# Kernel optimization log

Hardware: AMD Instinct MI355X
Metric: run time of the kernel (lower is better)

Reference implementation:

```python
import jax, jax.numpy as jnp
import numpy as np
import math

IN_DIM, OUT_DIM, NUM_BASIS = 256, 128, 6
MAX_IN_SEQ, MAX_OUT_SEQ = 512, 256
REDUCTION = 2
LN_EPS = 1e-5


def setup_inputs() -> dict:
    key = jax.random.key(0)
    ks = jax.random.split(key, 8)
    u = lambda k, shape, a: jax.random.uniform(k, shape, jnp.float32, -a, a)
    x = jax.random.normal(ks[0], (16, MAX_IN_SEQ, IN_DIM), jnp.float32)
    M = u(ks[1], (OUT_DIM, IN_DIM), 0.5)
    P = u(ks[2], (OUT_DIM, OUT_DIM, NUM_BASIS), 0.1)
    Linker = u(ks[3], (MAX_IN_SEQ, MAX_OUT_SEQ), 0.1)
    ln_gamma = jnp.ones((OUT_DIM,), jnp.float32)
    ln_beta = jnp.zeros((OUT_DIM,), jnp.float32)
    res_W = u(ks[4], (OUT_DIM, IN_DIM), 0.1)
    res_linker = u(ks[5], (MAX_IN_SEQ, MAX_OUT_SEQ), 0.1)
    # periods[i,j,g] = i*(out_dim*num_basis) + j*num_basis + g + 2 (non-trainable buffer)
    periods = (jnp.arange(OUT_DIM * OUT_DIM * NUM_BASIS, dtype=jnp.float32)
               .reshape(OUT_DIM, OUT_DIM, NUM_BASIS) + 2.0)
    return {"x": x, "M": M, "P": P, "Linker": Linker, "ln_gamma": ln_gamma,
            "ln_beta": ln_beta, "res_W": res_W, "res_linker": res_linker,
            "periods": periods, "actual_seq_len": 512}


def _layer_norm(z, gamma, beta):
    mu = jnp.mean(z, axis=-1, keepdims=True)
    var = jnp.var(z, axis=-1, keepdims=True)
    return (z - mu) * jax.lax.rsqrt(var + LN_EPS) * gamma + beta


def reference(x, M, P, Linker, ln_gamma, ln_beta, res_W, res_linker, periods, actual_seq_len):
    b, seq_len, _ = x.shape
    # Z = LN(x @ M^T)
    Z = _layer_norm(jnp.matmul(x, M.T), ln_gamma, ln_beta)  # (b, s, out)
    # position-dependent trig basis: phi[s,i,j,g] = cos(2*pi*s / periods[i,j,g])
    k = jnp.arange(seq_len, dtype=jnp.float32)[:, None, None, None]
    phi = jnp.cos(2.0 * math.pi * k / periods[None])          # (s, out, out, nb)
    # fold basis into per-position mixing matrix, then contract (matches sum over dims 3,4)
    W = jnp.einsum('ijg,sijg->sij', P, phi)                   # (s, out, out)
    T = jnp.einsum('bsj,sij->bsi', Z, W)                      # (b, s, out)
    # adaptive linker: reduce sequence length
    L = actual_seq_len
    Lo = max(1, L // REDUCTION)
    U = jnp.einsum('bsi,so->boi', T[:, :L], Linker[:L, :Lo])  # (b, out_seq, out)
    # 'separate' residual
    rfeat = jnp.matmul(x[:, :L], res_W.T)                     # (b, s, out)
    residual = jnp.einsum('bsi,so->boi', rfeat, res_linker[:L, :Lo])
    return U + residual
```

## Files before the change

### kernel.cpp

```cpp
#include <hip/hip_runtime.h>
#include <hip/hip_bf16.h>

#define LN_EPS 1e-5f


typedef __attribute__((ext_vector_type(8))) short short8;
typedef __attribute__((ext_vector_type(4))) float floatx4;

__device__ __forceinline__ unsigned short f2bf(float f) {
    __hip_bfloat16 h = __float2bfloat16(f);
    union { __hip_bfloat16 h; unsigned short u; } v; v.h = h; return v.u;
}
__device__ __forceinline__ unsigned int pack2(float a, float b) {
    return (unsigned int)f2bf(a) | ((unsigned int)f2bf(b) << 16);
}
__device__ __forceinline__ short8 pack8(float4 a, float4 b) {
    union { short8 s; uint4 u; } v;
    v.u.x = pack2(a.x, a.y); v.u.y = pack2(a.z, a.w);
    v.u.z = pack2(b.x, b.y); v.u.w = pack2(b.z, b.w);
    return v.s;
}

union SMem {
    struct { float buf[32 * 258]; float red1[256]; float red2[256]; float mus[32]; float rsg[32]; } p1;
    struct { unsigned short axs[32 * 40]; unsigned short bs[256 * 40]; } stg;
    unsigned short lcat[32 * 260];
};

__global__ __launch_bounds__(256) void s1_produce(const float* __restrict__ x,
                                                  const float* __restrict__ M,
                                                  const float* __restrict__ resW,
                                                  const float* __restrict__ gamma,
                                                  const float* __restrict__ beta,
                                                  const float* __restrict__ P,
                                                  const float* __restrict__ periods,
                                                  const float* __restrict__ Linker,
                                                  const float* __restrict__ resL,
                                                  unsigned short* __restrict__ Z,
                                                  unsigned short* __restrict__ TRt,
                                                  unsigned short* __restrict__ W,
                                                  unsigned short* __restrict__ LcatT) {
    __shared__ SMem sm;
    int blk = blockIdx.x, t = threadIdx.x;
    int w = t >> 6, l = t & 63;
    int lane15 = l & 15, quad = l >> 4;

    if (blk < 512) {
        int et = blk & 31, sc = blk >> 5;
        int n0 = et * 512 + t * 2;
        int jj = n0 & 7, il = (n0 >> 3) & 15, kq = (n0 >> 7) & 15, ig = (n0 >> 11) & 7;
        int e0 = (ig * 16 + il) * 128 + kq * 8 + jj;
        const float* pp = P + (size_t)e0 * 6;
        float4 pa = *(const float4*)(pp);
        float4 pb = *(const float4*)(pp + 4);
        float4 pc = *(const float4*)(pp + 8);
        float pf[12] = { pa.x, pa.y, pa.z, pa.w, pb.x, pb.y, pb.z, pb.w, pc.x, pc.y, pc.z, pc.w };
        const float* qp = periods + (size_t)e0 * 6;
        float4 qa = *(const float4*)(qp);
        float4 qb = *(const float4*)(qp + 4);
        float4 qc = *(const float4*)(qp + 8);
        float iv[12] = { __builtin_amdgcn_rcpf(qa.x), __builtin_amdgcn_rcpf(qa.y),
                         __builtin_amdgcn_rcpf(qa.z), __builtin_amdgcn_rcpf(qa.w),
                         __builtin_amdgcn_rcpf(qb.x), __builtin_amdgcn_rcpf(qb.y),
                         __builtin_amdgcn_rcpf(qb.z), __builtin_amdgcn_rcpf(qb.w),
                         __builtin_amdgcn_rcpf(qc.x), __builtin_amdgcn_rcpf(qc.y),
                         __builtin_amdgcn_rcpf(qc.z), __builtin_amdgcn_rcpf(qc.w) };
        float s0f = (float)(sc * 32);
        float tc[12], cm1[12], cc[12];
        #pragma unroll
        for (int g = 0; g < 12; ++g) {
            tc[g]  = 2.0f * __builtin_amdgcn_cosf(iv[g]);
            cm1[g] = __builtin_amdgcn_cosf(__builtin_amdgcn_fractf(s0f * iv[g]));
            cc[g]  = __builtin_amdgcn_cosf(__builtin_amdgcn_fractf((s0f + 1.0f) * iv[g]));
        }
        #pragma unroll 4
        for (int ss = 0; ss < 32; ++ss) {
            float a0 = 0.f, a1 = 0.f;
            #pragma unroll
            for (int g = 0; g < 6; ++g)  a0 += pf[g] * cm1[g];
            #pragma unroll
            for (int g = 6; g < 12; ++g) a1 += pf[g] * cm1[g];
            int s = sc * 32 + ss;
            *(unsigned int*)(W + (size_t)s * 16384 + n0) = pack2(a0, a1);
            #pragma unroll
            for (int g = 0; g < 12; ++g) {
                float cn = fmaf(tc[g], cc[g], -cm1[g]);
                cm1[g] = cc[g]; cc[g] = cn;
            }
        }
    } else if (blk < 768) {
        int r0 = (blk - 512) * 32;
        int wco = w * 64;
        floatx4 acc[2][4] = {};
        for (int km = 0; km < 256; km += 32) {
            {
                int row = t >> 3, c4 = (t & 7) * 4;
                float4 v = *(const float4*)(x + (size_t)(r0 + row) * 256 + km + c4);
                uint2 u; u.x = pack2(v.x, v.y); u.y = pack2(v.z, v.w);
                *(uint2*)(sm.stg.axs + row * 40 + c4) = u;
            }
            #pragma unroll
            for (int q = 0; q < 8; ++q) {
                int idx = t + 256 * q;
                int row = idx >> 3, c4 = (idx & 7) * 4;
                const float* src = (row < 128) ? (M + (size_t)row * 256)
                                               : (resW + (size_t)(row - 128) * 256);
                float4 v = *(const float4*)(src + km + c4);
                uint2 u; u.x = pack2(v.x, v.y); u.y = pack2(v.z, v.w);
                *(uint2*)(sm.stg.bs + row * 40 + c4) = u;
            }
            __syncthreads();
            int k0 = quad * 8;
            short8 a0 = *(const short8*)(sm.stg.axs + lane15 * 40 + k0);
            short8 a1 = *(const short8*)(sm.stg.axs + (16 + lane15) * 40 + k0);
            #pragma unroll
            for (int nt = 0; nt < 4; ++nt) {
                short8 b = *(const short8*)(sm.stg.bs + (wco + nt * 16 + lane15) * 40 + k0);
                acc[0][nt] = __builtin_amdgcn_mfma_f32_16x16x32_bf16(a0, b, acc[0][nt], 0, 0, 0);
                acc[1][nt] = __builtin_amdgcn_mfma_f32_16x16x32_bf16(a1, b, acc[1][nt], 0, 0, 0);
            }
            __syncthreads();
        }
        #pragma unroll
        for (int mt = 0; mt < 2; ++mt)
            #pragma unroll
            for (int nt = 0; nt < 4; ++nt)
                #pragma unroll
                for (int r = 0; r < 4; ++r) {
                    int ro = mt * 16 + quad * 4 + r;
                    int co = w * 64 + nt * 16 + lane15;
                    sm.p1.buf[ro * 258 + co] = acc[mt][nt][r];
                }
        __syncthreads();
        {
            int r = t >> 3, seg = t & 7;
            float s1 = 0.f, s2 = 0.f;
            #pragma unroll
            for (int e = 0; e < 16; ++e) { float v = sm.p1.buf[r * 258 + seg * 16 + e]; s1 += v; s2 += v * v; }
            sm.p1.red1[r * 8 + seg] = s1; sm.p1.red2[r * 8 + seg] = s2;
        }
        __syncthreads();
        if (t < 32) {
            float s1 = 0.f, s2 = 0.f;
            #pragma unroll
            for (int e = 0; e < 8; ++e) { s1 += sm.p1.red1[t * 8 + e]; s2 += sm.p1.red2[t * 8 + e]; }
            float mu = s1 * (1.0f / 128.0f);
            float var = s2 * (1.0f / 128.0f) - mu * mu;
            sm.p1.mus[t] = mu; sm.p1.rsg[t] = rsqrtf(var + LN_EPS);
        }
        __syncthreads();
        int b = r0 >> 9, s0 = r0 & 511;
        {
            int r = t >> 3, c0 = (t & 7) * 16;
            int s_t = s0 + r;
            float mu = sm.p1.mus[r], rs = sm.p1.rsg[r];
            float zv[16];
            #pragma unroll
            for (int e = 0; e < 16; ++e) {
                int j = c0 + e;
                zv[e] = (sm.p1.buf[r * 258 + j] - mu) * rs * gamma[j] + beta[j];
            }
            uint4 oz0, oz1;
            oz0.x = pack2(zv[0], zv[1]);  oz0.y = pack2(zv[2], zv[3]);
            oz0.z = pack2(zv[4], zv[5]);  oz0.w = pack2(zv[6], zv[7]);
            oz1.x = pack2(zv[8], zv[9]);  oz1.y = pack2(zv[10], zv[11]);
            oz1.z = pack2(zv[12], zv[13]); oz1.w = pack2(zv[14], zv[15]);
            unsigned short* zdst = Z + (size_t)s_t * 2048 + (((c0 >> 3) * 16 + b) << 3);
            *(uint4*)(zdst) = oz0;
            *(uint4*)(zdst + 128) = oz1;
        }
        {
            int j = t >> 1, sh = (t & 1) * 16;
            unsigned int ow[8];
            #pragma unroll
            for (int p = 0; p < 8; ++p) {
                float v0 = sm.p1.buf[(sh + 2 * p) * 258 + 128 + j];
                float v1 = sm.p1.buf[(sh + 2 * p + 1) * 258 + 128 + j];
                ow[p] = pack2(v0, v1);
            }
            int kqA = 64 + ((s0 + sh) >> 3);
            unsigned short* dst = TRt + (size_t)b * 131072 + ((size_t)(kqA * 128 + j) << 3);
            uint4 u0; u0.x = ow[0]; u0.y = ow[1]; u0.z = ow[2]; u0.w = ow[3];
            uint4 u1; u1.x = ow[4]; u1.y = ow[5]; u1.z = ow[6]; u1.w = ow[7];
            *(uint4*)(dst) = u0;
            *(uint4*)(dst + 1024) = u1;
        }
    } else {
        int kb = blk - 768;
        int k0 = kb * 32;
        const float* src = (kb < 16) ? (Linker + (size_t)k0 * 256)
                                     : (resL + (size_t)(k0 - 512) * 256);
        #pragma unroll
        for (int q = 0; q < 8; ++q) {
            int lin = t + 256 * q;
            int row = lin >> 6, col4 = (lin & 63) * 4;
            float4 v = *(const float4*)(src + row * 256 + col4);
            *(unsigned int*)(sm.lcat + row * 260 + col4)     = pack2(v.x, v.y);
            *(unsigned int*)(sm.lcat + row * 260 + col4 + 2) = pack2(v.z, v.w);
        }
        __syncthreads();
        int o = t;
        unsigned int outw[16];
        #pragma unroll
        for (int kp = 0; kp < 16; ++kp) {
            unsigned int lo = sm.lcat[(2 * kp) * 260 + o];
            unsigned int hi = sm.lcat[(2 * kp + 1) * 260 + o];
            outw[kp] = lo | (hi << 16);
        }
        #pragma unroll
        for (int qq = 0; qq < 4; ++qq) {
            uint4 u; u.x = outw[qq*4]; u.y = outw[qq*4+1]; u.z = outw[qq*4+2]; u.w = outw[qq*4+3];
            *(uint4*)(LcatT + (((size_t)(kb * 4 + qq) * 256 + o) << 3)) = u;
        }
    }
}

__global__ __launch_bounds__(256) void k2b_t(const unsigned short* __restrict__ W,
                                             const unsigned short* __restrict__ Z,
                                             unsigned short* __restrict__ TRt) {
    __shared__ unsigned short tbuf[16 * 64 * 4];
    int t = threadIdx.x, w = t >> 6, l = t & 63;
    int lane15 = l & 15, quad = l >> 4;
    int st = blockIdx.x >> 1, ih = blockIdx.x & 1;
    int s0 = st * 4;
    int ig = ih * 4 + w;
    #pragma unroll
    for (int ss = 0; ss < 4; ++ss) {
        int s = s0 + ss;
        floatx4 acc = {};
        #pragma unroll
        for (int kk = 0; kk < 4; ++kk) {
            int kq = kk * 4 + quad;
            short8 a  = *(const short8*)(Z + (size_t)s * 2048 + ((kq * 16 + lane15) << 3));
            short8 bf = *(const short8*)(W + (size_t)s * 16384 + (((ig * 16 + kq) * 16 + lane15) << 3));
            acc = __builtin_amdgcn_mfma_f32_16x16x32_bf16(a, bf, acc, 0, 0, 0);
        }
        int il = w * 16 + lane15;
        #pragma unroll
        for (int r = 0; r < 4; ++r) {
            int brow = quad * 4 + r;
            tbuf[(brow * 64 + il) * 4 + ss] = f2bf(acc[r]);
        }
    }
    __syncthreads();
    int ihb = ih * 64;
    #pragma unroll
    for (int q = 0; q < 4; ++q) {
        int p = t + 256 * q;
        int b = p >> 6, il = p & 63;
        uint2 v = *(const uint2*)(tbuf + p * 4);
        *(uint2*)(TRt + (size_t)b * 131072 + (((s0 >> 3) * 128 + ihb + il) << 3) + (s0 & 7)) = v;
    }
}

__global__ __launch_bounds__(256) void k3_out(const unsigned short* __restrict__ LcatT,
                                              const unsigned short* __restrict__ TRt,
                                              float* __restrict__ out) {
    __shared__ float red[4 * 32 * 64];
    int t = threadIdx.x, w = t >> 6, l = t & 63;
    int lane15 = l & 15, quad = l >> 4;
    int b = blockIdx.x, o0 = blockIdx.y * 32, i0 = blockIdx.z * 64;
    const unsigned short* trb = TRt + (size_t)b * 131072;
    floatx4 acc[2][4] = {};
    #pragma unroll 2
    for (int kk = 0; kk < 8; ++kk) {
        int k0 = w * 256 + kk * 32 + quad * 8;
        int kq = k0 >> 3;
        short8 afr0 = *(const short8*)(LcatT + (((size_t)kq * 256 + o0 + lane15) << 3));
        short8 afr1 = *(const short8*)(LcatT + (((size_t)kq * 256 + o0 + 16 + lane15) << 3));
        #pragma unroll
        for (int nt = 0; nt < 4; ++nt) {
            short8 bfr = *(const short8*)(trb + (((size_t)kq * 128 + i0 + nt * 16 + lane15) << 3));
            acc[0][nt] = __builtin_amdgcn_mfma_f32_16x16x32_bf16(afr0, bfr, acc[0][nt], 0, 0, 0);
            acc[1][nt] = __builtin_amdgcn_mfma_f32_16x16x32_bf16(afr1, bfr, acc[1][nt], 0, 0, 0);
        }
    }
    #pragma unroll
    for (int mt = 0; mt < 2; ++mt)
        #pragma unroll
        for (int nt = 0; nt < 4; ++nt)
            #pragma unroll
            for (int r = 0; r < 4; ++r) {
                int ro = mt * 16 + quad * 4 + r;
                int co = nt * 16 + lane15;
                red[(w * 32 + ro) * 64 + co] = acc[mt][nt][r];
            }
    __syncthreads();
    {
        int ro = t >> 3, c0 = (t & 7) * 8;
        float vs[8];
        #pragma unroll
        for (int e = 0; e < 8; ++e) {
            float sum = 0.f;
            #pragma unroll
            for (int ww = 0; ww < 4; ++ww) sum += red[(ww * 32 + ro) * 64 + c0 + e];
            vs[e] = sum;
        }
        float4 o1 = { vs[0], vs[1], vs[2], vs[3] };
        float4 o2 = { vs[4], vs[5], vs[6], vs[7] };
        size_t ob = ((size_t)b * 256 + o0 + ro) * 128 + i0 + c0;
        *(float4*)(out + ob) = o1;
        *(float4*)(out + ob + 4) = o2;
    }
}

extern "C" void kernel_launch(void* const* d_in, const int* in_sizes, int n_in,
                              void* d_out, int out_size, void* d_ws, size_t ws_size,
                              hipStream_t stream) {
    const float* x      = (const float*)d_in[0];
    const float* M      = (const float*)d_in[1];
    const float* P      = (const float*)d_in[2];
    const float* Linker = (const float*)d_in[3];
    const float* gamma  = (const float*)d_in[4];
    const float* beta   = (const float*)d_in[5];
    const float* resW   = (const float*)d_in[6];
    const float* resL   = (const float*)d_in[7];
    const float* periods= (const float*)d_in[8];
    (void)in_sizes; (void)n_in; (void)out_size; (void)ws_size;

    float* ws = (float*)d_ws;
    unsigned short* LcatT = (unsigned short*)(ws);
    unsigned short* Z     = (unsigned short*)(ws + 131072);
    unsigned short* TRt   = (unsigned short*)(ws + 655360);
    unsigned short* W     = (unsigned short*)(ws + 1703936);

    s1_produce<<<800, 256, 0, stream>>>(x, M, resW, gamma, beta, P, periods,
                                        Linker, resL, Z, TRt, W, LcatT);
    k2b_t<<<256, 256, 0, stream>>>(W, Z, TRt);
    k3_out<<<dim3(16, 8, 2), 256, 0, stream>>>(LcatT, TRt, (float*)d_out);
}
```

Measured before the change: 106.8 us.

## Fuse three kernels into one cooperative megakernel with grid syncs

Merges the producer, T-computation and output kernels into a single cooperative launch of 512 blocks separated by grid-wide barriers. Roles are reassigned: 256 blocks do the LN matmul while the other 256 build the linker transpose and each compute two W tiles. The goal is to remove launch gaps and inter-kernel drain. In exchange it adds grid.sync costs, leaves half the blocks idle in the later phases, and serialises more W work per block.

```diff
diff --git a/kernel.cpp b/kernel.cpp
--- a/kernel.cpp
+++ b/kernel.cpp
@@ -1,5 +1,8 @@
 #include <hip/hip_runtime.h>
 #include <hip/hip_bf16.h>
+#include <hip/hip_cooperative_groups.h>
+
+namespace cg = cooperative_groups;
 
 #define LN_EPS 1e-5f
 
@@ -13,215 +16,203 @@
 }
 __device__ __forceinline__ unsigned int pack2(float a, float b) {
     return (unsigned int)f2bf(a) | ((unsigned int)f2bf(b) << 16);
-}
-__device__ __forceinline__ short8 pack8(float4 a, float4 b) {
-    union { short8 s; uint4 u; } v;
-    v.u.x = pack2(a.x, a.y); v.u.y = pack2(a.z, a.w);
-    v.u.z = pack2(b.x, b.y); v.u.w = pack2(b.z, b.w);
-    return v.s;
 }
 
 union SMem {
     struct { float buf[32 * 258]; float red1[256]; float red2[256]; float mus[32]; float rsg[32]; } p1;
     struct { unsigned short axs[32 * 40]; unsigned short bs[256 * 40]; } stg;
     unsigned short lcat[32 * 260];
+    unsigned short tbuf[16 * 64 * 4];
+    float red[4 * 32 * 64];
 };
 
-__global__ __launch_bounds__(256) void s1_produce(const float* __restrict__ x,
-                                                  const float* __restrict__ M,
-                                                  const float* __restrict__ resW,
-                                                  const float* __restrict__ gamma,
-                                                  const float* __restrict__ beta,
-                                                  const float* __restrict__ P,
-                                                  const float* __restrict__ periods,
-                                                  const float* __restrict__ Linker,
-                                                  const float* __restrict__ resL,
-                                                  unsigned short* __restrict__ Z,
-                                                  unsigned short* __restrict__ TRt,
-                                                  unsigned short* __restrict__ W,
-                                                  unsigned short* __restrict__ LcatT) {
-    __shared__ SMem sm;
-    int blk = blockIdx.x, t = threadIdx.x;
+__device__ void role_w(int vb, int t, const float* __restrict__ P,
+                       const float* __restrict__ periods, unsigned short* __restrict__ W) {
+    int et = vb & 31, sc = vb >> 5;
+    int n0 = et * 512 + t * 2;
+    int jj = n0 & 7, il = (n0 >> 3) & 15, kq = (n0 >> 7) & 15, ig = (n0 >> 11) & 7;
+    int e0 = (ig * 16 + il) * 128 + kq * 8 + jj;
+    const float* pp = P + (size_t)e0 * 6;
+    float4 pa = *(const float4*)(pp);
+    float4 pb = *(const float4*)(pp + 4);
+    float4 pc = *(const float4*)(pp + 8);
+    float pf[12] = { pa.x, pa.y, pa.z, pa.w, pb.x, pb.y, pb.z, pb.w, pc.x, pc.y, pc.z, pc.w };
+    const float* qp = periods + (size_t)e0 * 6;
+    float4 qa = *(const float4*)(qp);
+    float4 qb = *(const float4*)(qp + 4);
+    float4 qc = *(const float4*)(qp + 8);
+    float iv[12] = { __builtin_amdgcn_rcpf(qa.x), __builtin_amdgcn_rcpf(qa.y),
+                     __builtin_amdgcn_rcpf(qa.z), __builtin_amdgcn_rcpf(qa.w),
+                     __builtin_amdgcn_rcpf(qb.x), __builtin_amdgcn_rcpf(qb.y),
+                     __builtin_amdgcn_rcpf(qb.z), __builtin_amdgcn_rcpf(qb.w),
+                     __builtin_amdgcn_rcpf(qc.x), __builtin_amdgcn_rcpf(qc.y),
+                     __builtin_amdgcn_rcpf(qc.z), __builtin_amdgcn_rcpf(qc.w) };
+    float s0f = (float)(sc * 32);
+    float tc[12], cm1[12], cc[12];
+    #pragma unroll
+    for (int g = 0; g < 12; ++g) {
+        tc[g]  = 2.0f * __builtin_amdgcn_cosf(iv[g]);
+        cm1[g] = __builtin_amdgcn_cosf(__builtin_amdgcn_fractf(s0f * iv[g]));
+        cc[g]  = __builtin_amdgcn_cosf(__builtin_amdgcn_fractf((s0f + 1.0f) * iv[g]));
+    }
+    #pragma unroll 4
+    for (int ss = 0; ss < 32; ++ss) {
+        float a0 = 0.f, a1 = 0.f;
+        #pragma unroll
+        for (int g = 0; g < 6; ++g)  a0 += pf[g] * cm1[g];
+        #pragma unroll
+        for (int g = 6; g < 12; ++g) a1 += pf[g] * cm1[g];
+        int s = sc * 32 + ss;
+        *(unsigned int*)(W + (size_t)s * 16384 + n0) = pack2(a0, a1);
+        #pragma unroll
+        for (int g = 0; g < 12; ++g) {
+            float cn = fmaf(tc[g], cc[g], -cm1[g]);
+            cm1[g] = cc[g]; cc[g] = cn;
+        }
+    }
+}
+
+__device__ void role_k1(SMem& sm, int vb, int t,
+                        const float* __restrict__ x, const float* __restrict__ M,
+                        const float* __restrict__ resW, const float* __restrict__ gamma,
+                        const float* __restrict__ beta,
+                        unsigned short* __restrict__ Z, unsigned short* __restrict__ TRt) {
     int w = t >> 6, l = t & 63;
     int lane15 = l & 15, quad = l >> 4;
-
-    if (blk < 512) {
-        int et = blk & 31, sc = blk >> 5;
-        int n0 = et * 512 + t * 2;
-        int jj = n0 & 7, il = (n0 >> 3) & 15, kq = (n0 >> 7) & 15, ig = (n0 >> 11) & 7;
-        int e0 = (ig * 16 + il) * 128 + kq * 8 + jj;
-        const float* pp = P + (size_t)e0 * 6;
-        float4 pa = *(const float4*)(pp);
-        float4 pb = *(const float4*)(pp + 4);
-        float4 pc = *(const float4*)(pp + 8);
-        float pf[12] = { pa.x, pa.y, pa.z, pa.w, pb.x, pb.y, pb.z, pb.w, pc.x, pc.y, pc.z, pc.w };
-        const float* qp = periods + (size_t)e0 * 6;
-        float4 qa = *(const float4*)(qp);
-        float4 qb = *(const float4*)(qp + 4);
-        float4 qc = *(const float4*)(qp + 8);
-        float iv[12] = { __builtin_amdgcn_rcpf(qa.x), __builtin_amdgcn_rcpf(qa.y),
-                         __builtin_amdgcn_rcpf(qa.z), __builtin_amdgcn_rcpf(qa.w),
-                         __builtin_amdgcn_rcpf(qb.x), __builtin_amdgcn_rcpf(qb.y),
-                         __builtin_amdgcn_rcpf(qb.z), __builtin_amdgcn_rcpf(qb.w),
-                         __builtin_amdgcn_rcpf(qc.x), __builtin_amdgcn_rcpf(qc.y),
-                         __builtin_amdgcn_rcpf(qc.z), __builtin_amdgcn_rcpf(qc.w) };
-        float s0f = (float)(sc * 32);
-        float tc[12], cm1[12], cc[12];
-        #pragma unroll
-        for (int g = 0; g < 12; ++g) {
-            tc[g]  = 2.0f * __builtin_amdgcn_cosf(iv[g]);
-            cm1[g] = __builtin_amdgcn_cosf(__builtin_amdgcn_fractf(s0f * iv[g]));
-            cc[g]  = __builtin_amdgcn_cosf(__builtin_amdgcn_fractf((s0f + 1.0f) * iv[g]));
-        }
-        #pragma unroll 4
-        for (int ss = 0; ss < 32; ++ss) {
-            float a0 = 0.f, a1 = 0.f;
+    int r0 = vb * 32;
+    int wco = w * 64;
+    floatx4 acc[2][4] = {};
+    for (int km = 0; km < 256; km += 32) {
+        {
+            int row = t >> 3, c4 = (t & 7) * 4;
+            float4 v = *(const float4*)(x + (size_t)(r0 + row) * 256 + km + c4);
+            uint2 u; u.x = pack2(v.x, v.y); u.y = pack2(v.z, v.w);
+            *(uint2*)(sm.stg.axs + row * 40 + c4) = u;
+        }
+        #pragma unroll
+        for (int q = 0; q < 8; ++q) {
+            int idx = t + 256 * q;
+            int row = idx >> 3, c4 = (idx & 7) * 4;
+            const float* src = (row < 128) ? (M + (size_t)row * 256)
+                                           : (resW + (size_t)(row - 128) * 256);
+            float4 v = *(const float4*)(src + km + c4);
+            uint2 u; u.x = pack2(v.x, v.y); u.y = pack2(v.z, v.w);
+            *(uint2*)(sm.stg.bs + row * 40 + c4) = u;
+        }
+        __syncthreads();
+        int k0 = quad * 8;
+        short8 a0 = *(const short8*)(sm.stg.axs + lane15 * 40 + k0);
+        short8 a1 = *(const short8*)(sm.stg.axs + (16 + lane15) * 40 + k0);
+        #pragma unroll
+        for (int nt = 0; nt < 4; ++nt) {
+            short8 b = *(const short8*)(sm.stg.bs + (wco + nt * 16 + lane15) * 40 + k0);
+            acc[0][nt] = __builtin_amdgcn_mfma_f32_16x16x32_bf16(a0, b, acc[0][nt], 0, 0, 0);
+            acc[1][nt] = __builtin_amdgcn_mfma_f32_16x16x32_bf16(a1, b, acc[1][nt], 0, 0, 0);
+        }
+        __syncthreads();
+    }
+    #pragma unroll
+    for (int mt = 0; mt < 2; ++mt)
+        #pragma unroll
+        for (int nt = 0; nt < 4; ++nt)
             #pragma unroll
-            for (int g = 0; g < 6; ++g)  a0 += pf[g] * cm1[g];
-            #pragma unroll
-            for (int g = 6; g < 12; ++g) a1 += pf[g] * cm1[g];
-            int s = sc * 32 + ss;
-            *(unsigned int*)(W + (size_t)s * 16384 + n0) = pack2(a0, a1);
-            #pragma unroll
-            for (int g = 0; g < 12; ++g) {
-                float cn = fmaf(tc[g], cc[g], -cm1[g]);
-                cm1[g] = cc[g]; cc[g] = cn;
+            for (int r = 0; r < 4; ++r) {
+                int ro = mt * 16 + quad * 4 + r;
+                int co = w * 64 + nt * 16 + lane15;
+                sm.p1.buf[ro * 258 + co] = acc[mt][nt][r];
             }
-        }
-    } else if (blk < 768) {
-        int r0 = (blk - 512) * 32;
-        int wco = w * 64;
-        floatx4 acc[2][4] = {};
-        for (int km = 0; km < 256; km += 32) {
-            {
-                int row = t >> 3, c4 = (t & 7) * 4;
-                float4 v = *(const float4*)(x + (size_t)(r0 + row) * 256 + km + c4);
-                uint2 u; u.x = pack2(v.x, v.y); u.y = pack2(v.z, v.w);
-                *(uint2*)(sm.stg.axs + row * 40 + c4) = u;
-            }
-            #pragma unroll
-            for (int q = 0; q < 8; ++q) {
-                int idx = t + 256 * q;
-                int row = idx >> 3, c4 = (idx & 7) * 4;
-                const float* src = (row < 128) ? (M + (size_t)row * 256)
-                                               : (resW + (size_t)(row - 128) * 256);
-                float4 v = *(const float4*)(src + km + c4);
-                uint2 u; u.x = pack2(v.x, v.y); u.y = pack2(v.z, v.w);
-                *(uint2*)(sm.stg.bs + row * 40 + c4) = u;
-            }
-            __syncthreads();
-            int k0 = quad * 8;
-            short8 a0 = *(const short8*)(sm.stg.axs + lane15 * 40 + k0);
-            short8 a1 = *(const short8*)(sm.stg.axs + (16 + lane15) * 40 + k0);
-            #pragma unroll
-            for (int nt = 0; nt < 4; ++nt) {
-                short8 b = *(const short8*)(sm.stg.bs + (wco + nt * 16 + lane15) * 40 + k0);
-                acc[0][nt] = __builtin_amdgcn_mfma_f32_16x16x32_bf16(a0, b, acc[0][nt], 0, 0, 0);
-                acc[1][nt] = __builtin_amdgcn_mfma_f32_16x16x32_bf16(a1, b, acc[1][nt], 0, 0, 0);
-            }
-            __syncthreads();
-        }
-        #pragma unroll
-        for (int mt = 0; mt < 2; ++mt)
-            #pragma unroll
-            for (int nt = 0; nt < 4; ++nt)
-                #pragma unroll
-                for (int r = 0; r < 4; ++r) {
-                    int ro = mt * 16 + quad * 4 + r;
-                    int co = w * 64 + nt * 16 + lane15;
-                    sm.p1.buf[ro * 258 + co] = acc[mt][nt][r];
-                }
-        __syncthreads();
-        {
-            int r = t >> 3, seg = t & 7;
-            float s1 = 0.f, s2 = 0.f;
-            #pragma unroll
-            for (int e = 0; e < 16; ++e) { float v = sm.p1.buf[r * 258 + seg * 16 + e]; s1 += v; s2 += v * v; }
-            sm.p1.red1[r * 8 + seg] = s1; sm.p1.red2[r * 8 + seg] = s2;
-        }
-        __syncthreads();
-        if (t < 32) {
-            float s1 = 0.f, s2 = 0.f;
-            #pragma unroll
-            for (int e = 0; e < 8; ++e) { s1 += sm.p1.red1[t * 8 + e]; s2 += sm.p1.red2[t * 8 + e]; }
-            float mu = s1 * (1.0f / 128.0f);
-            float var = s2 * (1.0f / 128.0f) - mu * mu;
-            sm.p1.mus[t] = mu; sm.p1.rsg[t] = rsqrtf(var + LN_EPS);
-        }
-        __syncthreads();
-        int b = r0 >> 9, s0 = r0 & 511;
-        {
-            int r = t >> 3, c0 = (t & 7) * 16;
-            int s_t = s0 + r;
-            float mu = sm.p1.mus[r], rs = sm.p1.rsg[r];
-            float zv[16];
-            #pragma unroll
-            for (int e = 0; e < 16; ++e) {
-                int j = c0 + e;
-                zv[e] = (sm.p1.buf[r * 258 + j] - mu) * rs * gamma[j] + beta[j];
-            }
-            uint4 oz0, oz1;
-            oz0.x = pack2(zv[0], zv[1]);  oz0.y = pack2(zv[2], zv[3]);
-            oz0.z = pack2(zv[4], zv[5]);  oz0.w = pack2(zv[6], zv[7]);
-            oz1.x = pack2(zv[8], zv[9]);  oz1.y = pack2(zv[10], zv[11]);
-            oz1.z = pack2(zv[12], zv[13]); oz1.w = pack2(zv[14], zv[15]);
-            unsigned short* zdst = Z + (size_t)s_t * 2048 + (((c0 >> 3) * 16 + b) << 3);
-            *(uint4*)(zdst) = oz0;
-            *(uint4*)(zdst + 128) = oz1;
-        }
-        {
-            int j = t >> 1, sh = (t & 1) * 16;
-            unsigned int ow[8];
-            #pragma unroll
-            for (int p = 0; p < 8; ++p) {
-                float v0 = sm.p1.buf[(sh + 2 * p) * 258 + 128 + j];
-                float v1 = sm.p1.buf[(sh + 2 * p + 1) * 258 + 128 + j];
-                ow[p] = pack2(v0, v1);
-            }
-            int kqA = 64 + ((s0 + sh) >> 3);
-            unsigned short* dst = TRt + (size_t)b * 131072 + ((size_t)(kqA * 128 + j) << 3);
-            uint4 u0; u0.x = ow[0]; u0.y = ow[1]; u0.z = ow[2]; u0.w = ow[3];
-            uint4 u1; u1.x = ow[4]; u1.y = ow[5]; u1.z = ow[6]; u1.w = ow[7];
-            *(uint4*)(dst) = u0;
-            *(uint4*)(dst + 1024) = u1;
-        }
-    } else {
-        int kb = blk - 768;
-        int k0 = kb * 32;
-        const float* src = (kb < 16) ? (Linker + (size_t)k0 * 256)
-                                     : (resL + (size_t)(k0 - 512) * 256);
-        #pragma unroll
-        for (int q = 0; q < 8; ++q) {
-            int lin = t + 256 * q;
-            int row = lin >> 6, col4 = (lin & 63) * 4;
-            float4 v = *(const float4*)(src + row * 256 + col4);
-            *(unsigned int*)(sm.lcat + row * 260 + col4)     = pack2(v.x, v.y);
-            *(unsigned int*)(sm.lcat + row * 260 + col4 + 2) = pack2(v.z, v.w);
-        }
-        __syncthreads();
-        int o = t;
-        unsigned int outw[16];
-        #pragma unroll
-        for (int kp = 0; kp < 16; ++kp) {
-            unsigned int lo = sm.lcat[(2 * kp) * 260 + o];
-            unsigned int hi = sm.lcat[(2 * kp + 1) * 260 + o];
-            outw[kp] = lo | (hi << 16);
-        }
-        #pragma unroll
-        for (int qq = 0; qq < 4; ++qq) {
-            uint4 u; u.x = outw[qq*4]; u.y = outw[qq*4+1]; u.z = outw[qq*4+2]; u.w = outw[qq*4+3];
-            *(uint4*)(LcatT + (((size_t)(kb * 4 + qq) * 256 + o) << 3)) = u;
-        }
-    }
-}
-
-__global__ __launch_bounds__(256) void k2b_t(const unsigned short* __restrict__ W,
-                                             const unsigned short* __restrict__ Z,
-                                             unsigned short* __restrict__ TRt) {
-    __shared__ unsigned short tbuf[16 * 64 * 4];
-    int t = threadIdx.x, w = t >> 6, l = t & 63;
+    __syncthreads();
+    {
+        int r = t >> 3, seg = t & 7;
+        float s1 = 0.f, s2 = 0.f;
+        #pragma unroll
+        for (int e = 0; e < 16; ++e) { float v = sm.p1.buf[r * 258 + seg * 16 + e]; s1 += v; s2 += v * v; }
+        sm.p1.red1[r * 8 + seg] = s1; sm.p1.red2[r * 8 + seg] = s2;
+    }
+    __syncthreads();
+    if (t < 32) {
+        float s1 = 0.f, s2 = 0.f;
+        #pragma unroll
+        for (int e = 0; e < 8; ++e) { s1 += sm.p1.red1[t * 8 + e]; s2 += sm.p1.red2[t * 8 + e]; }
+        float mu = s1 * (1.0f / 128.0f);
+        float var = s2 * (1.0f / 128.0f) - mu * mu;
+        sm.p1.mus[t] = mu; sm.p1.rsg[t] = rsqrtf(var + LN_EPS);
+    }
+    __syncthreads();
+    int b = r0 >> 9, s0 = r0 & 511;
+    {
+        int r = t >> 3, c0 = (t & 7) * 16;
+        int s_t = s0 + r;
+        float mu = sm.p1.mus[r], rs = sm.p1.rsg[r];
+        float zv[16];
+        #pragma unroll
+        for (int e = 0; e < 16; ++e) {
+            int j = c0 + e;
+            zv[e] = (sm.p1.buf[r * 258 + j] - mu) * rs * gamma[j] + beta[j];
+        }
+        uint4 oz0, oz1;
+        oz0.x = pack2(zv[0], zv[1]);  oz0.y = pack2(zv[2], zv[3]);
+        oz0.z = pack2(zv[4], zv[5]);  oz0.w = pack2(zv[6], zv[7]);
+        oz1.x = pack2(zv[8], zv[9]);  oz1.y = pack2(zv[10], zv[11]);
+        oz1.z = pack2(zv[12], zv[13]); oz1.w = pack2(zv[14], zv[15]);
+        unsigned short* zdst = Z + (size_t)s_t * 2048 + (((c0 >> 3) * 16 + b) << 3);
+        *(uint4*)(zdst) = oz0;
+        *(uint4*)(zdst + 128) = oz1;
+    }
+    {
+        int j = t >> 1, sh = (t & 1) * 16;
+        unsigned int ow[8];
+        #pragma unroll
+        for (int p = 0; p < 8; ++p) {
+            float v0 = sm.p1.buf[(sh + 2 * p) * 258 + 128 + j];
+            float v1 = sm.p1.buf[(sh + 2 * p + 1) * 258 + 128 + j];
+            ow[p] = pack2(v0, v1);
+        }
+        int kqA = 64 + ((s0 + sh) >> 3);
+        unsigned short* dst = TRt + (size_t)b * 131072 + ((size_t)(kqA * 128 + j) << 3);
+        uint4 u0; u0.x = ow[0]; u0.y = ow[1]; u0.z = ow[2]; u0.w = ow[3];
+        uint4 u1; u1.x = ow[4]; u1.y = ow[5]; u1.z = ow[6]; u1.w = ow[7];
+        *(uint4*)(dst) = u0;
+        *(uint4*)(dst + 1024) = u1;
+    }
+}
+
+__device__ void role_lc(SMem& sm, int vb, int t, const float* __restrict__ Linker,
+                        const float* __restrict__ resL, unsigned short* __restrict__ LcatT) {
+    int kb = vb;
+    int k0 = kb * 32;
+    const float* src = (kb < 16) ? (Linker + (size_t)k0 * 256)
+                                 : (resL + (size_t)(k0 - 512) * 256);
+    #pragma unroll
+    for (int q = 0; q < 8; ++q) {
+        int lin = t + 256 * q;
+        int row = lin >> 6, col4 = (lin & 63) * 4;
+        float4 v = *(const float4*)(src + row * 256 + col4);
+        *(unsigned int*)(sm.lcat + row * 260 + col4)     = pack2(v.x, v.y);
+        *(unsigned int*)(sm.lcat + row * 260 + col4 + 2) = pack2(v.z, v.w);
+    }
+    __syncthreads();
+    int o = t;
+    unsigned int outw[16];
+    #pragma unroll
+    for (int kp = 0; kp < 16; ++kp) {
+        unsigned int lo = sm.lcat[(2 * kp) * 260 + o];
+        unsigned int hi = sm.lcat[(2 * kp + 1) * 260 + o];
+        outw[kp] = lo | (hi << 16);
+    }
+    #pragma unroll
+    for (int qq = 0; qq < 4; ++qq) {
+        uint4 u; u.x = outw[qq*4]; u.y = outw[qq*4+1]; u.z = outw[qq*4+2]; u.w = outw[qq*4+3];
+        *(uint4*)(LcatT + (((size_t)(kb * 4 + qq) * 256 + o) << 3)) = u;
+    }
+    __syncthreads();
+}
+
+__device__ void role_k2b(SMem& sm, int vb, int t, const unsigned short* __restrict__ W,
+                         const unsigned short* __restrict__ Z, unsigned short* __restrict__ TRt) {
+    int w = t >> 6, l = t & 63;
     int lane15 = l & 15, quad = l >> 4;
-    int st = blockIdx.x >> 1, ih = blockIdx.x & 1;
+    int st = vb >> 1, ih = vb & 1;
     int s0 = st * 4;
     int ig = ih * 4 + w;
     #pragma unroll
@@ -239,7 +230,7 @@
         #pragma unroll
         for (int r = 0; r < 4; ++r) {
             int brow = quad * 4 + r;
-            tbuf[(brow * 64 + il) * 4 + ss] = f2bf(acc[r]);
+            sm.tbuf[(brow * 64 + il) * 4 + ss] = f2bf(acc[r]);
         }
     }
     __syncthreads();
@@ -248,18 +239,16 @@
     for (int q = 0; q < 4; ++q) {
         int p = t + 256 * q;
         int b = p >> 6, il = p & 63;
-        uint2 v = *(const uint2*)(tbuf + p * 4);
+        uint2 v = *(const uint2*)(sm.tbuf + p * 4);
         *(uint2*)(TRt + (size_t)b * 131072 + (((s0 >> 3) * 128 + ihb + il) << 3) + (s0 & 7)) = v;
     }
 }
 
-__global__ __launch_bounds__(256) void k3_out(const unsigned short* __restrict__ LcatT,
-                                              const unsigned short* __restrict__ TRt,
-                                              float* __restrict__ out) {
-    __shared__ float red[4 * 32 * 64];
-    int t = threadIdx.x, w = t >> 6, l = t & 63;
+__device__ void role_k3(SMem& sm, int vb, int t, const unsigned short* __restrict__ LcatT,
+                        const unsigned short* __restrict__ TRt, float* __restrict__ out) {
+    int w = t >> 6, l = t & 63;
     int lane15 = l & 15, quad = l >> 4;
-    int b = blockIdx.x, o0 = blockIdx.y * 32, i0 = blockIdx.z * 64;
+    int b = vb & 15, o0 = ((vb >> 4) & 7) * 32, i0 = (vb >> 7) * 64;
     const unsigned short* trb = TRt + (size_t)b * 131072;
     floatx4 acc[2][4] = {};
     #pragma unroll 2
@@ -283,7 +272,7 @@
             for (int r = 0; r < 4; ++r) {
                 int ro = mt * 16 + quad * 4 + r;
                 int co = nt * 16 + lane15;
-                red[(w * 32 + ro) * 64 + co] = acc[mt][nt][r];
+                sm.red[(w * 32 + ro) * 64 + co] = acc[mt][nt][r];
             }
     __syncthreads();
     {
@@ -293,7 +282,7 @@
         for (int e = 0; e < 8; ++e) {
             float sum = 0.f;
             #pragma unroll
-            for (int ww = 0; ww < 4; ++ww) sum += red[(ww * 32 + ro) * 64 + c0 + e];
+            for (int ww = 0; ww < 4; ++ww) sum += sm.red[(ww * 32 + ro) * 64 + c0 + e];
             vs[e] = sum;
         }
         float4 o1 = { vs[0], vs[1], vs[2], vs[3] };
@@ -302,6 +291,40 @@
         *(float4*)(out + ob) = o1;
         *(float4*)(out + ob + 4) = o2;
     }
+}
+
+__global__ __launch_bounds__(256, 2) void mega(const float* __restrict__ x,
+                                               const float* __restrict__ M,
+                                               const float* __restrict__ resW,
+                                               const float* __restrict__ gamma,
+                                               const float* __restrict__ beta,
+                                               const float* __restrict__ P,
+                                               const float* __restrict__ periods,
+                                               const float* __restrict__ Linker,
+                                               const float* __restrict__ resL,
+                                               unsigned short* __restrict__ Z,
+                                               unsigned short* __restrict__ TRt,
+                                               unsigned short* __restrict__ W,
+                                               unsigned short* __restrict__ LcatT,
+                                               float* __restrict__ out) {
+    __shared__ SMem sm;
+    cg::grid_group grid = cg::this_grid();
+    int blk = blockIdx.x, t = threadIdx.x;
+
+    if (blk < 256) {
+        role_k1(sm, blk, t, x, M, resW, gamma, beta, Z, TRt);
+    } else {
+        if (blk < 288) role_lc(sm, blk - 256, t, Linker, resL, LcatT);
+        int v0 = (blk - 256) * 2;
+        role_w(v0, t, P, periods, W);
+        role_w(v0 + 1, t, P, periods, W);
+    }
+    grid.sync();
+
+    if (blk < 256) role_k2b(sm, blk, t, W, Z, TRt);
+    grid.sync();
+
+    if (blk < 256) role_k3(sm, blk, t, LcatT, TRt, out);
 }
 
 extern "C" void kernel_launch(void* const* d_in, const int* in_sizes, int n_in,
@@ -323,9 +346,10 @@
     unsigned short* Z     = (unsigned short*)(ws + 131072);
     unsigned short* TRt   = (unsigned short*)(ws + 655360);
     unsigned short* W     = (unsigned short*)(ws + 1703936);
-
-    s1_produce<<<800, 256, 0, stream>>>(x, M, resW, gamma, beta, P, periods,
-                                        Linker, resL, Z, TRt, W, LcatT);
-    k2b_t<<<256, 256, 0, stream>>>(W, Z, TRt);
-    k3_out<<<dim3(16, 8, 2), 256, 0, stream>>>(LcatT, TRt, (float*)d_out);
-}
+    float* outp = (float*)d_out;
+
+    void* args[] = { (void*)&x, (void*)&M, (void*)&resW, (void*)&gamma, (void*)&beta,
+                     (void*)&P, (void*)&periods, (void*)&Linker, (void*)&resL,
+                     (void*)&Z, (void*)&TRt, (void*)&W, (void*)&LcatT, (void*)&outp };
+    hipLaunchCooperativeKernel((const void*)mega, dim3(512), dim3(256), args, 0, stream);
+}
```

New measurement: 242.0 us. 2.27x slower.
